# Performance work log

Hardware: AMD Instinct MI355X
Metric: run time of the kernel (lower is better)

The kernel has to match this reference:

```python
import jax, jax.numpy as jnp
import numpy as np

LOG_2PI = float(np.log(2.0 * np.pi))


def setup_inputs() -> dict:
    key = jax.random.key(0)
    k1, k2, k3 = jax.random.split(key, 3)
    B, T, F, K = 16, 1024, 1024, 500
    X = jax.random.normal(k1, (B, T, F), dtype=jnp.float32)
    mu = jax.random.normal(k2, (K, F), dtype=jnp.float32)
    # cov must be positive for log(cov); uniform in [0.5, 1.5)
    cov = jax.random.uniform(k3, (K, F), dtype=jnp.float32) + 0.5
    return {"X": X, "mu": mu, "cov": cov}


def reference(X, mu, cov):
    # Diagonal-covariance GMM log-likelihoods: out[b,t,k] = log N(X[b,t]; mu[k], diag(cov[k]))
    # Algebraic expansion of 0.5*sum((x-mu)^2/cov) into two GEMMs + bias, avoiding
    # the BxTxKxF broadcast intermediate. Same math as the torch module.
    D = mu.shape[-1]
    inv_cov = 1.0 / cov                                   # (K, F)
    C = -0.5 * D * LOG_2PI - 0.5 * jnp.sum(jnp.log(cov), axis=-1)  # (K,)
    quad = jnp.einsum('btf,kf->btk', X * X, inv_cov)      # sum x^2/cov
    cross = jnp.einsum('btf,kf->btk', X, mu * inv_cov)    # sum x*mu/cov
    const = jnp.sum(mu * mu * inv_cov, axis=-1)           # (K,) sum mu^2/cov
    ULL = 0.5 * (quad - 2.0 * cross + const[None, None, :])
    return C[None, None, :] - ULL                         # (B, T, K)
```

## Files before the change

### kernel.cpp

```cpp
#include <hip/hip_runtime.h>
#include <hip/hip_bf16.h>


typedef __attribute__((ext_vector_type(8))) __bf16 bf16x8;
typedef __attribute__((ext_vector_type(4))) float  f32x4;

#define LOG_2PI 1.837877066409345339082f

constexpr int M_TOT = 16384;
constexpr int F_DIM = 1024;
constexpr int K_GMM = 500;
constexpr int N_PAD = 512;

constexpr int BM  = 128;
constexpr int BN  = 128;
constexpr int BKF = 32;
constexpr int NIT = F_DIM / BKF;

__device__ __forceinline__ unsigned pack_sq_x(float x) {
    __hip_bfloat162 h = __float22bfloat162_rn(make_float2(x * x, x));
    union { __hip_bfloat162 h; unsigned u; } cv;
    cv.h = h;
    return cv.u;
}

__global__ __launch_bounds__(256) void prep_w_kernel(
    const float* __restrict__ mu, const float* __restrict__ cov,
    unsigned* __restrict__ Wimg, float* __restrict__ bias)
{
    const int k = blockIdx.x;
    const int t = threadIdx.x;
    const int tt  = k >> 7;
    const int wch = (k >> 6) & 1;
    const int b   = (k >> 4) & 3;
    const int lo  = k & 15;
    float sl = 0.f, sq = 0.f;
    #pragma unroll
    for (int j = 0; j < 4; ++j) {
        const int d  = t + j * 256;
        const int it = d >> 5;
        const int c  = (d >> 4) & 1;
        const int hi = (d >> 2) & 3;
        const int jj = d & 3;
        const int dw = ((((tt * 2 + wch) * 32 + it) * 8) + (b * 2 + c)) * 256
                     + (hi * 16 + lo) * 4 + jj;
        if (k < K_GMM) {
            const float cv_ = cov[k * F_DIM + d];
            const float m_  = mu[k * F_DIM + d];
            const float ic  = 1.0f / cv_;
            __hip_bfloat162 h = __float22bfloat162_rn(make_float2(-0.5f * ic, m_ * ic));
            union { __hip_bfloat162 h; unsigned u; } cvt; cvt.h = h;
            Wimg[dw] = cvt.u;
            sl += logf(cv_);
            sq += m_ * m_ * ic;
        } else {
            Wimg[dw] = 0u;
        }
    }
    #pragma unroll
    for (int off = 32; off > 0; off >>= 1) {
        sl += __shfl_down(sl, off, 64);
        sq += __shfl_down(sq, off, 64);
    }
    __shared__ float red[8];
    if ((t & 63) == 0) { red[(t >> 6) * 2] = sl; red[(t >> 6) * 2 + 1] = sq; }
    __syncthreads();
    if (t == 0) {
        const float SL = red[0] + red[2] + red[4] + red[6];
        const float SQ = red[1] + red[3] + red[5] + red[7];
        bias[k] = (k < K_GMM)
                ? (-0.5f * (F_DIM * LOG_2PI) - 0.5f * SL - 0.5f * SQ) : 0.f;
    }
}

__global__ __launch_bounds__(256, 2) void gemm_kernel(
    const float* __restrict__ X, const unsigned* __restrict__ Wimg,
    const float* __restrict__ bias, float* __restrict__ out)
{
    __shared__ __align__(16) char smem[32768];
    float* ep = reinterpret_cast<float*>(smem);

    const int bid    = blockIdx.x;
    const int m_base = (bid & 127) * BM;
    const int n_tile = bid >> 7;
    const int n_base = n_tile * BN;

    const int tid  = threadIdx.x;
    const int lane = tid & 63;
    const int wv   = tid >> 6;
    const int wr   = (wv >> 1) * 64;
    const int wch  = wv & 1;
    const int wc   = wch * 64;
    const int hi   = lane >> 4;
    const int lo   = lane & 15;
    const int lsw  = lo & 7;

    const int sr = tid >> 1;
    const int sh = tid & 1;

    const float4* Xv = reinterpret_cast<const float4*>(X);
    const bf16x8* Wf = reinterpret_cast<const bf16x8*>(Wimg);
    const int wbase = (n_tile * 2 + wch) * 32 * 8 * 64;

    f32x4 acc[4][4];
    #pragma unroll
    for (int a = 0; a < 4; ++a)
        #pragma unroll
        for (int b = 0; b < 4; ++b)
            acc[a][b] = (f32x4){0.f, 0.f, 0.f, 0.f};

    auto loadA = [&](int itS, float4* ar) {
        #pragma unroll
        for (int j = 0; j < 4; ++j)
            ar[j] = Xv[(m_base + sr) * (F_DIM / 4) + itS * 8 + sh * 4 + j];
    };
    auto packA = [&](const float4* ar, int ab) {
        unsigned short* Ad = reinterpret_cast<unsigned short*>(smem + ab * 16384);
        #pragma unroll
        for (int j = 0; j < 4; ++j) {
            const int chunk = (sh * 4 + j) ^ (sr & 7);
            uint4 wa;
            wa.x = pack_sq_x(ar[j].x);
            wa.y = pack_sq_x(ar[j].y);
            wa.z = pack_sq_x(ar[j].z);
            wa.w = pack_sq_x(ar[j].w);
            *reinterpret_cast<uint4*>(&Ad[sr * 64 + chunk * 8]) = wa;
        }
    };
    auto loadB = [&](int itS, bf16x8* br) {
        #pragma unroll
        for (int f = 0; f < 8; ++f)
            br[f] = Wf[wbase + (itS * 8 + f) * 64 + lane];
    };
    auto mfmas = [&](int ab, const bf16x8* br) {
        const unsigned short* Asc =
            reinterpret_cast<const unsigned short*>(smem + ab * 16384);
        bf16x8 af[4];
        __builtin_amdgcn_s_setprio(1);
        #pragma unroll
        for (int c = 0; c < 2; ++c) {
            #pragma unroll
            for (int a = 0; a < 4; ++a) {
                const int row   = wr + a * 16 + lo;
                const int chunk = (c * 4 + hi) ^ lsw;
                af[a] = *reinterpret_cast<const bf16x8*>(&Asc[row * 64 + chunk * 8]);
            }
            #pragma unroll
            for (int a = 0; a < 4; ++a)
                #pragma unroll
                for (int b = 0; b < 4; ++b)
                    acc[a][b] = __builtin_amdgcn_mfma_f32_16x16x32_bf16(
                        af[a], br[b * 2 + c], acc[a][b], 0, 0, 0);
        }
        __builtin_amdgcn_s_setprio(0);
    };

    float4 aA[4], aB[4];
    bf16x8 b0[8], b1[8];
    loadA(0, aA);
    loadB(0, b0);
    loadA(1, aB);
    loadB(1, b1);
    packA(aA, 0);
    loadA(2, aA);
    asm volatile("s_waitcnt lgkmcnt(0)" ::: "memory");
    __builtin_amdgcn_s_barrier();
    __builtin_amdgcn_sched_barrier(0);

    for (int it = 0; it < NIT; it += 2) {
        packA(aB, 1);
        if (it + 3 < NIT) loadA(it + 3, aB);
        mfmas(0, b0);
        if (it + 2 < NIT) loadB(it + 2, b0);
        asm volatile("s_waitcnt lgkmcnt(0)" ::: "memory");
        __builtin_amdgcn_s_barrier();
        __builtin_amdgcn_sched_barrier(0);

        if (it + 2 < NIT) packA(aA, 0);
        if (it + 4 < NIT) loadA(it + 4, aA);
        mfmas(1, b1);
        if (it + 3 < NIT) loadB(it + 3, b1);
        asm volatile("s_waitcnt lgkmcnt(0)" ::: "memory");
        __builtin_amdgcn_s_barrier();
        __builtin_amdgcn_sched_barrier(0);
    }

    const int ncols = (K_GMM - n_base < BN) ? (K_GMM - n_base) : BN;
    #pragma unroll
    for (int p = 0; p < 2; ++p) {
        if (p) __syncthreads();
        if ((wv >> 1) == p) {
            #pragma unroll
            for (int b = 0; b < 4; ++b) {
                const int col = wc + b * 16 + lo;
                const float bv = bias[n_base + col];
                #pragma unroll
                for (int a = 0; a < 4; ++a)
                    #pragma unroll
                    for (int i = 0; i < 4; ++i)
                        ep[(a * 16 + hi * 4 + i) * 128 + col] = acc[a][b][i] + bv;
            }
        }
        __syncthreads();
        #pragma unroll
        for (int k = 0; k < 8; ++k) {
            const int f    = k * 256 + tid;
            const int row  = f >> 5;
            const int slot = f & 31;
            if (slot * 4 < ncols) {
                const float4 v = *reinterpret_cast<const float4*>(&ep[row * 128 + slot * 4]);
                *reinterpret_cast<float4*>(
                    &out[(size_t)(m_base + p * 64 + row) * K_GMM + n_base + slot * 4]) = v;
            }
        }
    }
}

extern "C" void kernel_launch(void* const* d_in, const int* in_sizes, int n_in,
                              void* d_out, int out_size, void* d_ws, size_t ws_size,
                              hipStream_t stream)
{
    (void)in_sizes; (void)n_in; (void)out_size; (void)ws_size;
    const float* X   = (const float*)d_in[0];
    const float* mu  = (const float*)d_in[1];
    const float* cov = (const float*)d_in[2];
    float* out = (float*)d_out;

    unsigned* Wimg = (unsigned*)d_ws;
    float*    bias = (float*)((char*)d_ws + (size_t)N_PAD * F_DIM * 4);

    prep_w_kernel<<<dim3(N_PAD), dim3(256), 0, stream>>>(mu, cov, Wimg, bias);
    gemm_kernel<<<dim3((M_TOT / BM) * (N_PAD / BN)), dim3(256), 0, stream>>>(X, Wimg, bias, out);
}
```

Before: 56.11 us.

## Give each wave private A rows to drop block barriers in GEMM loop

Changes the wave tiling from 2x2 (64 rows by 64 columns per wave) to 4x1 (32 rows by all 128 columns per wave). Each wave now loads, packs and reads only its own A rows in a private LDS region, so the per-iteration s_barriers and lgkmcnt waits are removed. The epilogue also becomes per-wave staging without cross-wave sync. In exchange each wave loads twice as many B fragments from global memory per k-step and shared memory doubles to 64KB, which may lower occupancy.

```diff
diff --git a/kernel.cpp b/kernel.cpp
--- a/kernel.cpp
+++ b/kernel.cpp
@@ -77,8 +77,7 @@
     const float* __restrict__ X, const unsigned* __restrict__ Wimg,
     const float* __restrict__ bias, float* __restrict__ out)
 {
-    __shared__ __align__(16) char smem[32768];
-    float* ep = reinterpret_cast<float*>(smem);
+    __shared__ __align__(16) char smem[65536];
 
     const int bid    = blockIdx.x;
     const int m_base = (bid & 127) * BM;
@@ -88,130 +87,122 @@
     const int tid  = threadIdx.x;
     const int lane = tid & 63;
     const int wv   = tid >> 6;
-    const int wr   = (wv >> 1) * 64;
-    const int wch  = wv & 1;
-    const int wc   = wch * 64;
+    const int wrb  = wv * 32;
     const int hi   = lane >> 4;
     const int lo   = lane & 15;
     const int lsw  = lo & 7;
 
-    const int sr = tid >> 1;
-    const int sh = tid & 1;
+    const int lr = lane >> 1;
+    const int sh = lane & 1;
+    const int sr = wrb + lr;
 
     const float4* Xv = reinterpret_cast<const float4*>(X);
     const bf16x8* Wf = reinterpret_cast<const bf16x8*>(Wimg);
-    const int wbase = (n_tile * 2 + wch) * 32 * 8 * 64;
-
-    f32x4 acc[4][4];
-    #pragma unroll
-    for (int a = 0; a < 4; ++a)
-        #pragma unroll
-        for (int b = 0; b < 4; ++b)
+    const int wb0 = (n_tile * 2 + 0) * 32 * 8 * 64;
+    const int wb1 = (n_tile * 2 + 1) * 32 * 8 * 64;
+
+    f32x4 acc[2][8];
+    #pragma unroll
+    for (int a = 0; a < 2; ++a)
+        #pragma unroll
+        for (int b = 0; b < 8; ++b)
             acc[a][b] = (f32x4){0.f, 0.f, 0.f, 0.f};
 
     auto loadA = [&](int itS, float4* ar) {
         #pragma unroll
         for (int j = 0; j < 4; ++j)
-            ar[j] = Xv[(m_base + sr) * (F_DIM / 4) + itS * 8 + sh * 4 + j];
+            ar[j] = Xv[(size_t)(m_base + sr) * (F_DIM / 4) + itS * 8 + sh * 4 + j];
     };
     auto packA = [&](const float4* ar, int ab) {
-        unsigned short* Ad = reinterpret_cast<unsigned short*>(smem + ab * 16384);
+        unsigned short* Ad =
+            reinterpret_cast<unsigned short*>(smem + wv * 8192 + ab * 4096);
         #pragma unroll
         for (int j = 0; j < 4; ++j) {
-            const int chunk = (sh * 4 + j) ^ (sr & 7);
+            const int chunk = (sh * 4 + j) ^ (lr & 7);
             uint4 wa;
             wa.x = pack_sq_x(ar[j].x);
             wa.y = pack_sq_x(ar[j].y);
             wa.z = pack_sq_x(ar[j].z);
             wa.w = pack_sq_x(ar[j].w);
-            *reinterpret_cast<uint4*>(&Ad[sr * 64 + chunk * 8]) = wa;
-        }
-    };
-    auto loadB = [&](int itS, bf16x8* br) {
-        #pragma unroll
-        for (int f = 0; f < 8; ++f)
-            br[f] = Wf[wbase + (itS * 8 + f) * 64 + lane];
-    };
-    auto mfmas = [&](int ab, const bf16x8* br) {
+            *reinterpret_cast<uint4*>(&Ad[lr * 64 + chunk * 8]) = wa;
+        }
+    };
+    auto loadB = [&](int itS, int c, bf16x8* br) {
+        #pragma unroll
+        for (int b = 0; b < 4; ++b)
+            br[b] = Wf[wb0 + (itS * 8 + b * 2 + c) * 64 + lane];
+        #pragma unroll
+        for (int b = 0; b < 4; ++b)
+            br[4 + b] = Wf[wb1 + (itS * 8 + b * 2 + c) * 64 + lane];
+    };
+    auto mfma_c = [&](int ab, int c, const bf16x8* br) {
         const unsigned short* Asc =
-            reinterpret_cast<const unsigned short*>(smem + ab * 16384);
-        bf16x8 af[4];
+            reinterpret_cast<const unsigned short*>(smem + wv * 8192 + ab * 4096);
+        bf16x8 af[2];
+        #pragma unroll
+        for (int a = 0; a < 2; ++a) {
+            const int row   = a * 16 + lo;
+            const int chunk = (c * 4 + hi) ^ lsw;
+            af[a] = *reinterpret_cast<const bf16x8*>(&Asc[row * 64 + chunk * 8]);
+        }
         __builtin_amdgcn_s_setprio(1);
         #pragma unroll
-        for (int c = 0; c < 2; ++c) {
+        for (int a = 0; a < 2; ++a)
             #pragma unroll
-            for (int a = 0; a < 4; ++a) {
-                const int row   = wr + a * 16 + lo;
-                const int chunk = (c * 4 + hi) ^ lsw;
-                af[a] = *reinterpret_cast<const bf16x8*>(&Asc[row * 64 + chunk * 8]);
-            }
+            for (int b = 0; b < 8; ++b)
+                acc[a][b] = __builtin_amdgcn_mfma_f32_16x16x32_bf16(
+                    af[a], br[b], acc[a][b], 0, 0, 0);
+        __builtin_amdgcn_s_setprio(0);
+    };
+
+    float4 aA[4], aB[4];
+    bf16x8 bc0[8], bc1[8];
+    loadA(0, aA);
+    loadB(0, 0, bc0);
+    loadB(0, 1, bc1);
+    loadA(1, aB);
+    packA(aA, 0);
+
+    for (int it = 0; it < NIT; it += 2) {
+        if (it + 2 < NIT) loadA(it + 2, aA);
+        packA(aB, 1);
+        mfma_c(0, 0, bc0);
+        if (it + 1 < NIT) loadB(it + 1, 0, bc0);
+        mfma_c(0, 1, bc1);
+        if (it + 1 < NIT) loadB(it + 1, 1, bc1);
+
+        if (it + 3 < NIT) loadA(it + 3, aB);
+        if (it + 2 < NIT) packA(aA, 0);
+        mfma_c(1, 0, bc0);
+        if (it + 2 < NIT) loadB(it + 2, 0, bc0);
+        mfma_c(1, 1, bc1);
+        if (it + 2 < NIT) loadB(it + 2, 1, bc1);
+    }
+
+    __syncthreads();
+    float* epw = reinterpret_cast<float*>(smem + wv * 16384);
+    #pragma unroll
+    for (int b = 0; b < 8; ++b) {
+        const int col = b * 16 + lo;
+        const float bv = bias[n_base + col];
+        #pragma unroll
+        for (int a = 0; a < 2; ++a) {
+            const int er = a * 16 + hi * 4;
             #pragma unroll
-            for (int a = 0; a < 4; ++a)
-                #pragma unroll
-                for (int b = 0; b < 4; ++b)
-                    acc[a][b] = __builtin_amdgcn_mfma_f32_16x16x32_bf16(
-                        af[a], br[b * 2 + c], acc[a][b], 0, 0, 0);
-        }
-        __builtin_amdgcn_s_setprio(0);
-    };
-
-    float4 aA[4], aB[4];
-    bf16x8 b0[8], b1[8];
-    loadA(0, aA);
-    loadB(0, b0);
-    loadA(1, aB);
-    loadB(1, b1);
-    packA(aA, 0);
-    loadA(2, aA);
-    asm volatile("s_waitcnt lgkmcnt(0)" ::: "memory");
-    __builtin_amdgcn_s_barrier();
-    __builtin_amdgcn_sched_barrier(0);
-
-    for (int it = 0; it < NIT; it += 2) {
-        packA(aB, 1);
-        if (it + 3 < NIT) loadA(it + 3, aB);
-        mfmas(0, b0);
-        if (it + 2 < NIT) loadB(it + 2, b0);
-        asm volatile("s_waitcnt lgkmcnt(0)" ::: "memory");
-        __builtin_amdgcn_s_barrier();
-        __builtin_amdgcn_sched_barrier(0);
-
-        if (it + 2 < NIT) packA(aA, 0);
-        if (it + 4 < NIT) loadA(it + 4, aA);
-        mfmas(1, b1);
-        if (it + 3 < NIT) loadB(it + 3, b1);
-        asm volatile("s_waitcnt lgkmcnt(0)" ::: "memory");
-        __builtin_amdgcn_s_barrier();
-        __builtin_amdgcn_sched_barrier(0);
-    }
-
+            for (int i = 0; i < 4; ++i)
+                epw[(er + i) * 128 + col] = acc[a][b][i] + bv;
+        }
+    }
     const int ncols = (K_GMM - n_base < BN) ? (K_GMM - n_base) : BN;
-    #pragma unroll
-    for (int p = 0; p < 2; ++p) {
-        if (p) __syncthreads();
-        if ((wv >> 1) == p) {
-            #pragma unroll
-            for (int b = 0; b < 4; ++b) {
-                const int col = wc + b * 16 + lo;
-                const float bv = bias[n_base + col];
-                #pragma unroll
-                for (int a = 0; a < 4; ++a)
-                    #pragma unroll
-                    for (int i = 0; i < 4; ++i)
-                        ep[(a * 16 + hi * 4 + i) * 128 + col] = acc[a][b][i] + bv;
-            }
-        }
-        __syncthreads();
-        #pragma unroll
-        for (int k = 0; k < 8; ++k) {
-            const int f    = k * 256 + tid;
-            const int row  = f >> 5;
-            const int slot = f & 31;
-            if (slot * 4 < ncols) {
-                const float4 v = *reinterpret_cast<const float4*>(&ep[row * 128 + slot * 4]);
-                *reinterpret_cast<float4*>(
-                    &out[(size_t)(m_base + p * 64 + row) * K_GMM + n_base + slot * 4]) = v;
-            }
+    const int r2   = lane >> 5;
+    const int slot = lane & 31;
+    if (slot * 4 < ncols) {
+        #pragma unroll
+        for (int rr = 0; rr < 16; ++rr) {
+            const int row = rr * 2 + r2;
+            const float4 v = *reinterpret_cast<const float4*>(&epw[row * 128 + slot * 4]);
+            *reinterpret_cast<float4*>(
+                &out[(size_t)(m_base + wrb + row) * K_GMM + n_base + slot * 4]) = v;
         }
     }
 }
```

Result: slower. 66.60 us (+18.7%).

## Double K-step to 64 per barrier and write full epilogue tile at once

Applied to the files above, without the earlier changes.

Each main-loop iteration now covers 64 features instead of 32, using 32KB A buffers (64KB LDS total) with a 16-way XOR swizzle. This halves the number of barriers and lets one A pack overlap four MFMA phases. The epilogue stages the whole 128x128 tile in one pass rather than two half-tile passes, which removes a sync. In exchange, LDS per block doubles, so only one block of 256 threads may fit per CU instead of two, and aA now needs 8 float4 registers per thread.

```diff
diff --git a/kernel.cpp b/kernel.cpp
--- a/kernel.cpp
+++ b/kernel.cpp
@@ -14,7 +14,7 @@
 
 constexpr int BM  = 128;
 constexpr int BN  = 128;
-constexpr int BKF = 32;
+constexpr int BKF = 64;
 constexpr int NIT = F_DIM / BKF;
 
 __device__ __forceinline__ unsigned pack_sq_x(float x) {
@@ -37,12 +37,12 @@
     float sl = 0.f, sq = 0.f;
     #pragma unroll
     for (int j = 0; j < 4; ++j) {
-        const int d  = t + j * 256;
-        const int it = d >> 5;
-        const int c  = (d >> 4) & 1;
-        const int hi = (d >> 2) & 3;
-        const int jj = d & 3;
-        const int dw = ((((tt * 2 + wch) * 32 + it) * 8) + (b * 2 + c)) * 256
+        const int d   = t + j * 256;
+        const int blk = d >> 5;
+        const int c   = (d >> 4) & 1;
+        const int hi  = (d >> 2) & 3;
+        const int jj  = d & 3;
+        const int dw = ((((tt * 2 + wch) * 32 + blk) * 8) + (b * 2 + c)) * 256
                      + (hi * 16 + lo) * 4 + jj;
         if (k < K_GMM) {
             const float cv_ = cov[k * F_DIM + d];
@@ -77,8 +77,7 @@
     const float* __restrict__ X, const unsigned* __restrict__ Wimg,
     const float* __restrict__ bias, float* __restrict__ out)
 {
-    __shared__ __align__(16) char smem[32768];
-    float* ep = reinterpret_cast<float*>(smem);
+    __shared__ __align__(16) char smem[65536];
 
     const int bid    = blockIdx.x;
     const int m_base = (bid & 127) * BM;
@@ -93,7 +92,6 @@
     const int wc   = wch * 64;
     const int hi   = lane >> 4;
     const int lo   = lane & 15;
-    const int lsw  = lo & 7;
 
     const int sr = tid >> 1;
     const int sh = tid & 1;
@@ -109,109 +107,103 @@
         for (int b = 0; b < 4; ++b)
             acc[a][b] = (f32x4){0.f, 0.f, 0.f, 0.f};
 
-    auto loadA = [&](int itS, float4* ar) {
-        #pragma unroll
-        for (int j = 0; j < 4; ++j)
-            ar[j] = Xv[(m_base + sr) * (F_DIM / 4) + itS * 8 + sh * 4 + j];
+    auto loadA = [&](int kS, float4* ar) {
+        #pragma unroll
+        for (int j = 0; j < 8; ++j)
+            ar[j] = Xv[(size_t)(m_base + sr) * (F_DIM / 4) + kS * 16 + sh * 8 + j];
     };
     auto packA = [&](const float4* ar, int ab) {
-        unsigned short* Ad = reinterpret_cast<unsigned short*>(smem + ab * 16384);
-        #pragma unroll
-        for (int j = 0; j < 4; ++j) {
-            const int chunk = (sh * 4 + j) ^ (sr & 7);
+        unsigned short* Ad = reinterpret_cast<unsigned short*>(smem + ab * 32768);
+        #pragma unroll
+        for (int j = 0; j < 8; ++j) {
+            const int chunk = (sh * 8 + j) ^ (sr & 15);
             uint4 wa;
             wa.x = pack_sq_x(ar[j].x);
             wa.y = pack_sq_x(ar[j].y);
             wa.z = pack_sq_x(ar[j].z);
             wa.w = pack_sq_x(ar[j].w);
-            *reinterpret_cast<uint4*>(&Ad[sr * 64 + chunk * 8]) = wa;
-        }
-    };
-    auto loadB = [&](int itS, bf16x8* br) {
+            *reinterpret_cast<uint4*>(&Ad[sr * 128 + chunk * 8]) = wa;
+        }
+    };
+    auto loadB_blk = [&](int blk, bf16x8* br) {
         #pragma unroll
         for (int f = 0; f < 8; ++f)
-            br[f] = Wf[wbase + (itS * 8 + f) * 64 + lane];
-    };
-    auto mfmas = [&](int ab, const bf16x8* br) {
+            br[f] = Wf[wbase + (blk * 8 + f) * 64 + lane];
+    };
+    auto phase = [&](int ab, int s, const bf16x8* br) {
         const unsigned short* Asc =
-            reinterpret_cast<const unsigned short*>(smem + ab * 16384);
+            reinterpret_cast<const unsigned short*>(smem + ab * 32768);
+        const int c     = s & 1;
+        const int chunk = (s * 4 + hi) ^ lo;
         bf16x8 af[4];
+        #pragma unroll
+        for (int a = 0; a < 4; ++a) {
+            const int row = wr + a * 16 + lo;
+            af[a] = *reinterpret_cast<const bf16x8*>(&Asc[row * 128 + chunk * 8]);
+        }
         __builtin_amdgcn_s_setprio(1);
         #pragma unroll
-        for (int c = 0; c < 2; ++c) {
+        for (int a = 0; a < 4; ++a)
             #pragma unroll
-            for (int a = 0; a < 4; ++a) {
-                const int row   = wr + a * 16 + lo;
-                const int chunk = (c * 4 + hi) ^ lsw;
-                af[a] = *reinterpret_cast<const bf16x8*>(&Asc[row * 64 + chunk * 8]);
-            }
-            #pragma unroll
-            for (int a = 0; a < 4; ++a)
-                #pragma unroll
-                for (int b = 0; b < 4; ++b)
-                    acc[a][b] = __builtin_amdgcn_mfma_f32_16x16x32_bf16(
-                        af[a], br[b * 2 + c], acc[a][b], 0, 0, 0);
-        }
+            for (int b = 0; b < 4; ++b)
+                acc[a][b] = __builtin_amdgcn_mfma_f32_16x16x32_bf16(
+                    af[a], br[b * 2 + c], acc[a][b], 0, 0, 0);
         __builtin_amdgcn_s_setprio(0);
     };
 
-    float4 aA[4], aB[4];
+    float4 aA[8];
     bf16x8 b0[8], b1[8];
     loadA(0, aA);
-    loadB(0, b0);
-    loadA(1, aB);
-    loadB(1, b1);
+    loadB_blk(0, b0);
+    loadB_blk(1, b1);
     packA(aA, 0);
-    loadA(2, aA);
+    loadA(1, aA);
     asm volatile("s_waitcnt lgkmcnt(0)" ::: "memory");
     __builtin_amdgcn_s_barrier();
     __builtin_amdgcn_sched_barrier(0);
 
-    for (int it = 0; it < NIT; it += 2) {
-        packA(aB, 1);
-        if (it + 3 < NIT) loadA(it + 3, aB);
-        mfmas(0, b0);
-        if (it + 2 < NIT) loadB(it + 2, b0);
+    for (int k = 0; k < NIT; ++k) {
+        const int ab = k & 1;
+        if (k + 1 < NIT) {
+            packA(aA, ab ^ 1);
+            if (k + 2 < NIT) loadA(k + 2, aA);
+        }
+        phase(ab, 0, b0);
+        phase(ab, 1, b0);
+        if (k + 1 < NIT) loadB_blk(2 * (k + 1), b0);
+        phase(ab, 2, b1);
+        phase(ab, 3, b1);
+        if (k + 1 < NIT) loadB_blk(2 * (k + 1) + 1, b1);
         asm volatile("s_waitcnt lgkmcnt(0)" ::: "memory");
         __builtin_amdgcn_s_barrier();
         __builtin_amdgcn_sched_barrier(0);
-
-        if (it + 2 < NIT) packA(aA, 0);
-        if (it + 4 < NIT) loadA(it + 4, aA);
-        mfmas(1, b1);
-        if (it + 3 < NIT) loadB(it + 3, b1);
-        asm volatile("s_waitcnt lgkmcnt(0)" ::: "memory");
-        __builtin_amdgcn_s_barrier();
-        __builtin_amdgcn_sched_barrier(0);
-    }
+    }
+
+    float* ep = reinterpret_cast<float*>(smem);
+    #pragma unroll
+    for (int b = 0; b < 4; ++b) {
+        const int col = wc + b * 16 + lo;
+        const float bv = bias[n_base + col];
+        #pragma unroll
+        for (int a = 0; a < 4; ++a) {
+            const int er = wr + a * 16 + hi * 4;
+            #pragma unroll
+            for (int i = 0; i < 4; ++i)
+                ep[(er + i) * 128 + col] = acc[a][b][i] + bv;
+        }
+    }
+    __syncthreads();
 
     const int ncols = (K_GMM - n_base < BN) ? (K_GMM - n_base) : BN;
     #pragma unroll
-    for (int p = 0; p < 2; ++p) {
-        if (p) __syncthreads();
-        if ((wv >> 1) == p) {
-            #pragma unroll
-            for (int b = 0; b < 4; ++b) {
-                const int col = wc + b * 16 + lo;
-                const float bv = bias[n_base + col];
-                #pragma unroll
-                for (int a = 0; a < 4; ++a)
-                    #pragma unroll
-                    for (int i = 0; i < 4; ++i)
-                        ep[(a * 16 + hi * 4 + i) * 128 + col] = acc[a][b][i] + bv;
-            }
-        }
-        __syncthreads();
-        #pragma unroll
-        for (int k = 0; k < 8; ++k) {
-            const int f    = k * 256 + tid;
-            const int row  = f >> 5;
-            const int slot = f & 31;
-            if (slot * 4 < ncols) {
-                const float4 v = *reinterpret_cast<const float4*>(&ep[row * 128 + slot * 4]);
-                *reinterpret_cast<float4*>(
-                    &out[(size_t)(m_base + p * 64 + row) * K_GMM + n_base + slot * 4]) = v;
-            }
+    for (int q = 0; q < 16; ++q) {
+        const int f    = q * 256 + tid;
+        const int row  = f >> 5;
+        const int slot = f & 31;
+        if (slot * 4 < ncols) {
+            const float4 v = *reinterpret_cast<const float4*>(&ep[row * 128 + slot * 4]);
+            *reinterpret_cast<float4*>(
+                &out[(size_t)(m_base + row) * K_GMM + n_base + slot * 4]) = v;
         }
     }
 }
```

Result: slower. 66.45 us (+18.4%).

## Halve N tile to 64, single-buffer B registers, simplify epilogue

Applied to the files above, without the earlier changes.

Shrinks the GEMM N tile from 128 to 64 columns, so each wave computes a 64x32 sub-tile with half the accumulators and B registers. The grid doubles to 1024 blocks, the weight image layout in the prep kernel is rearranged to match, and the unrolled-by-two main loop becomes a single-step loop with one B register set. The aim is lower register pressure, higher occupancy and more blocks for load balance. In exchange, each X tile is re-read and re-packed twice as often (8 N tiles instead of 4), and B prefetch distance drops to one iteration.

```diff
diff --git a/kernel.cpp b/kernel.cpp
--- a/kernel.cpp
+++ b/kernel.cpp
@@ -13,7 +13,7 @@
 constexpr int N_PAD = 512;
 
 constexpr int BM  = 128;
-constexpr int BN  = 128;
+constexpr int BN  = 64;
 constexpr int BKF = 32;
 constexpr int NIT = F_DIM / BKF;
 
@@ -30,10 +30,9 @@
 {
     const int k = blockIdx.x;
     const int t = threadIdx.x;
-    const int tt  = k >> 7;
-    const int wch = (k >> 6) & 1;
-    const int b   = (k >> 4) & 3;
-    const int lo  = k & 15;
+    const int tt = k >> 6;
+    const int b  = (k >> 4) & 3;
+    const int lo = k & 15;
     float sl = 0.f, sq = 0.f;
     #pragma unroll
     for (int j = 0; j < 4; ++j) {
@@ -42,7 +41,7 @@
         const int c  = (d >> 4) & 1;
         const int hi = (d >> 2) & 3;
         const int jj = d & 3;
-        const int dw = ((((tt * 2 + wch) * 32 + it) * 8) + (b * 2 + c)) * 256
+        const int dw = ((tt * 32 + it) * 8 + (b * 2 + c)) * 256
                      + (hi * 16 + lo) * 4 + jj;
         if (k < K_GMM) {
             const float cv_ = cov[k * F_DIM + d];
@@ -89,8 +88,8 @@
     const int lane = tid & 63;
     const int wv   = tid >> 6;
     const int wr   = (wv >> 1) * 64;
-    const int wch  = wv & 1;
-    const int wc   = wch * 64;
+    const int wc   = (wv & 1) * 32;
+    const int wcb  = wc >> 4;
     const int hi   = lane >> 4;
     const int lo   = lane & 15;
     const int lsw  = lo & 7;
@@ -100,19 +99,19 @@
 
     const float4* Xv = reinterpret_cast<const float4*>(X);
     const bf16x8* Wf = reinterpret_cast<const bf16x8*>(Wimg);
-    const int wbase = (n_tile * 2 + wch) * 32 * 8 * 64;
-
-    f32x4 acc[4][4];
+    const int wbase = n_tile * 32 * 8 * 64;
+
+    f32x4 acc[4][2];
     #pragma unroll
     for (int a = 0; a < 4; ++a)
         #pragma unroll
-        for (int b = 0; b < 4; ++b)
+        for (int b = 0; b < 2; ++b)
             acc[a][b] = (f32x4){0.f, 0.f, 0.f, 0.f};
 
     auto loadA = [&](int itS, float4* ar) {
         #pragma unroll
         for (int j = 0; j < 4; ++j)
-            ar[j] = Xv[(m_base + sr) * (F_DIM / 4) + itS * 8 + sh * 4 + j];
+            ar[j] = Xv[(size_t)(m_base + sr) * (F_DIM / 4) + itS * 8 + sh * 4 + j];
     };
     auto packA = [&](const float4* ar, int ab) {
         unsigned short* Ad = reinterpret_cast<unsigned short*>(smem + ab * 16384);
@@ -129,89 +128,81 @@
     };
     auto loadB = [&](int itS, bf16x8* br) {
         #pragma unroll
-        for (int f = 0; f < 8; ++f)
-            br[f] = Wf[wbase + (itS * 8 + f) * 64 + lane];
+        for (int bi = 0; bi < 2; ++bi)
+            #pragma unroll
+            for (int c = 0; c < 2; ++c)
+                br[bi * 2 + c] = Wf[wbase + (itS * 8 + (wcb + bi) * 2 + c) * 64 + lane];
     };
     auto mfmas = [&](int ab, const bf16x8* br) {
         const unsigned short* Asc =
             reinterpret_cast<const unsigned short*>(smem + ab * 16384);
-        bf16x8 af[4];
-        __builtin_amdgcn_s_setprio(1);
         #pragma unroll
         for (int c = 0; c < 2; ++c) {
+            bf16x8 af[4];
             #pragma unroll
             for (int a = 0; a < 4; ++a) {
                 const int row   = wr + a * 16 + lo;
                 const int chunk = (c * 4 + hi) ^ lsw;
                 af[a] = *reinterpret_cast<const bf16x8*>(&Asc[row * 64 + chunk * 8]);
             }
+            __builtin_amdgcn_s_setprio(1);
             #pragma unroll
             for (int a = 0; a < 4; ++a)
                 #pragma unroll
-                for (int b = 0; b < 4; ++b)
+                for (int b = 0; b < 2; ++b)
                     acc[a][b] = __builtin_amdgcn_mfma_f32_16x16x32_bf16(
                         af[a], br[b * 2 + c], acc[a][b], 0, 0, 0);
-        }
-        __builtin_amdgcn_s_setprio(0);
-    };
-
-    float4 aA[4], aB[4];
-    bf16x8 b0[8], b1[8];
+            __builtin_amdgcn_s_setprio(0);
+        }
+    };
+
+    float4 aA[4];
+    bf16x8 bb[4];
     loadA(0, aA);
-    loadB(0, b0);
-    loadA(1, aB);
-    loadB(1, b1);
+    loadB(0, bb);
     packA(aA, 0);
-    loadA(2, aA);
+    loadA(1, aA);
     asm volatile("s_waitcnt lgkmcnt(0)" ::: "memory");
     __builtin_amdgcn_s_barrier();
     __builtin_amdgcn_sched_barrier(0);
 
-    for (int it = 0; it < NIT; it += 2) {
-        packA(aB, 1);
-        if (it + 3 < NIT) loadA(it + 3, aB);
-        mfmas(0, b0);
-        if (it + 2 < NIT) loadB(it + 2, b0);
+    for (int it = 0; it < NIT; ++it) {
+        const int ab = it & 1;
+        if (it + 1 < NIT) {
+            packA(aA, ab ^ 1);
+            if (it + 2 < NIT) loadA(it + 2, aA);
+        }
+        mfmas(ab, bb);
+        if (it + 1 < NIT) loadB(it + 1, bb);
         asm volatile("s_waitcnt lgkmcnt(0)" ::: "memory");
         __builtin_amdgcn_s_barrier();
         __builtin_amdgcn_sched_barrier(0);
-
-        if (it + 2 < NIT) packA(aA, 0);
-        if (it + 4 < NIT) loadA(it + 4, aA);
-        mfmas(1, b1);
-        if (it + 3 < NIT) loadB(it + 3, b1);
-        asm volatile("s_waitcnt lgkmcnt(0)" ::: "memory");
-        __builtin_amdgcn_s_barrier();
-        __builtin_amdgcn_sched_barrier(0);
-    }
+    }
+
+    #pragma unroll
+    for (int b = 0; b < 2; ++b) {
+        const int col = wc + b * 16 + lo;
+        const float bv = bias[n_base + col];
+        #pragma unroll
+        for (int a = 0; a < 4; ++a) {
+            const int er = wr + a * 16 + hi * 4;
+            #pragma unroll
+            for (int i = 0; i < 4; ++i)
+                ep[(er + i) * 64 + col] = acc[a][b][i] + bv;
+        }
+    }
+    __syncthreads();
 
     const int ncols = (K_GMM - n_base < BN) ? (K_GMM - n_base) : BN;
     #pragma unroll
-    for (int p = 0; p < 2; ++p) {
-        if (p) __syncthreads();
-        if ((wv >> 1) == p) {
-            #pragma unroll
-            for (int b = 0; b < 4; ++b) {
-                const int col = wc + b * 16 + lo;
-                const float bv = bias[n_base + col];
-                #pragma unroll
-                for (int a = 0; a < 4; ++a)
-                    #pragma unroll
-                    for (int i = 0; i < 4; ++i)
-                        ep[(a * 16 + hi * 4 + i) * 128 + col] = acc[a][b][i] + bv;
-            }
-        }
-        __syncthreads();
-        #pragma unroll
-        for (int k = 0; k < 8; ++k) {
-            const int f    = k * 256 + tid;
-            const int row  = f >> 5;
-            const int slot = f & 31;
-            if (slot * 4 < ncols) {
-                const float4 v = *reinterpret_cast<const float4*>(&ep[row * 128 + slot * 4]);
-                *reinterpret_cast<float4*>(
-                    &out[(size_t)(m_base + p * 64 + row) * K_GMM + n_base + slot * 4]) = v;
-            }
+    for (int q = 0; q < 8; ++q) {
+        const int f    = q * 256 + tid;
+        const int row  = f >> 4;
+        const int slot = f & 15;
+        if (slot * 4 < ncols) {
+            const float4 v = *reinterpret_cast<const float4*>(&ep[row * 64 + slot * 4]);
+            *reinterpret_cast<float4*>(
+                &out[(size_t)(m_base + row) * K_GMM + n_base + slot * 4]) = v;
         }
     }
 }
```

New measurement: 66.44 us. 1.18x slower.
